# Optimization experiments

Hardware: AMD Instinct MI355X
Metric: run time of the kernel (lower is better)

The kernel has to match this reference:

```python
import jax, jax.numpy as jnp
import numpy as np

N_NODES = 100000


def gcn_conv(x, src, dst, W, b):
    # x: [N, F_in]; src/dst: [E'] (self-loops already appended)
    n = x.shape[0]
    deg = jax.ops.segment_sum(jnp.ones_like(src, dtype=x.dtype), dst, num_segments=n)
    dinv = jnp.where(deg > 0, jax.lax.rsqrt(deg), 0.0)
    norm = dinv[src] * dinv[dst]                      # [E']
    h = x @ W                                         # [N, F_out] (GEMM first: F_out small)
    msg = h[src] * norm[:, None]                      # gather + scale
    out = jax.ops.segment_sum(msg, dst, num_segments=n)  # scatter-add
    return out + b


def setup_inputs() -> dict:
    key = jax.random.key(0)
    k1, k2, k3, k4 = jax.random.split(key, 4)
    x = jax.random.normal(k1, (N_NODES, 1433), dtype=jnp.float32)
    edge_index = jax.random.randint(k2, (2, 3200000), 0, N_NODES, dtype=jnp.int32)
    W1 = jax.random.normal(k3, (1433, 32), dtype=jnp.float32) * (1.0 / np.sqrt(1433.0))
    b1 = jnp.zeros((32,), dtype=jnp.float32)
    W2 = jax.random.normal(k4, (32, 7), dtype=jnp.float32) * (1.0 / np.sqrt(32.0))
    b2 = jnp.zeros((7,), dtype=jnp.float32)
    return {"x": x, "edge_index": edge_index, "W1": W1, "b1": b1, "W2": W2, "b2": b2}


def reference(x, edge_index, W1, b1, W2, b2):
    n = x.shape[0]
    loop = jnp.arange(n, dtype=edge_index.dtype)      # add self-loops (GCNConv default)
    src = jnp.concatenate([edge_index[0], loop])
    dst = jnp.concatenate([edge_index[1], loop])
    h = gcn_conv(x, src, dst, W1, b1)
    h = jax.nn.relu(h)
    # F.dropout with training=False (eval mode) is identity
    h = gcn_conv(h, src, dst, W2, b2)
    return jax.nn.log_softmax(h, axis=1)
```

## Files before the change

kernel.cpp:

```cpp
#include <hip/hip_runtime.h>
#include <math.h>

#define F0 1433
#define F1 32
#define F2 7

__global__ void k_init_deg(float* __restrict__ deg, int N) {
    int i = blockIdx.x * 256 + threadIdx.x;
    if (i < N) deg[i] = 1.0f;
}

__global__ void k_count_deg(const int* __restrict__ dst, float* __restrict__ deg, int E) {
    int e = blockIdx.x * 256 + threadIdx.x;
    if (e < E) atomicAdd(&deg[dst[e]], 1.0f);
}

__global__ void k_dinv(float* __restrict__ deg, int N) {
    int i = blockIdx.x * 256 + threadIdx.x;
    if (i < N) deg[i] = rsqrtf(deg[i]);
}

#define BM 64
#define BK 64
#define XS_LD 68
__global__ __launch_bounds__(256) void k_gemm1(const float* __restrict__ x,
                                               const float* __restrict__ W,
                                               float* __restrict__ h, int N) {
    __shared__ float xs[BM * XS_LD];
    __shared__ float wsm[BK * F1];
    const int tid  = threadIdx.x;
    const int row0 = blockIdx.x * BM;
    const int cg   = tid & 7;
    const int r    = tid >> 3;

    float acc0x = 0.f, acc0y = 0.f, acc0z = 0.f, acc0w = 0.f;
    float acc1x = 0.f, acc1y = 0.f, acc1z = 0.f, acc1w = 0.f;

    for (int k0 = 0; k0 < F0; k0 += BK) {
        #pragma unroll
        for (int l = 0; l < 16; ++l) {
            int idx = tid + l * 256;
            int i = idx >> 6, j = idx & 63;
            int gr = row0 + i, gk = k0 + j;
            float v = 0.f;
            if (gr < N && gk < F0) v = x[(long)gr * F0 + gk];
            xs[i * XS_LD + j] = v;
        }
        #pragma unroll
        for (int l = 0; l < 8; ++l) {
            int idx = tid + l * 256;
            int kk = idx >> 5;
            int gk = k0 + kk;
            wsm[idx] = (gk < F0) ? W[gk * F1 + (idx & 31)] : 0.f;
        }
        __syncthreads();

        #pragma unroll
        for (int kk = 0; kk < BK; kk += 4) {
            float4 xa = *(const float4*)&xs[r * XS_LD + kk];
            float4 xb = *(const float4*)&xs[(r + 32) * XS_LD + kk];
            const float av[4] = {xa.x, xa.y, xa.z, xa.w};
            const float bv[4] = {xb.x, xb.y, xb.z, xb.w};
            #pragma unroll
            for (int u = 0; u < 4; ++u) {
                float4 w = *(const float4*)&wsm[(kk + u) * F1 + cg * 4];
                float a = av[u], b = bv[u];
                acc0x += a * w.x; acc0y += a * w.y; acc0z += a * w.z; acc0w += a * w.w;
                acc1x += b * w.x; acc1y += b * w.y; acc1z += b * w.z; acc1w += b * w.w;
            }
        }
        __syncthreads();
    }
    int gr0 = row0 + r, gr1 = row0 + r + 32;
    if (gr0 < N) *(float4*)&h[(long)gr0 * F1 + cg * 4] = make_float4(acc0x, acc0y, acc0z, acc0w);
    if (gr1 < N) *(float4*)&h[(long)gr1 * F1 + cg * 4] = make_float4(acc1x, acc1y, acc1z, acc1w);
}

__global__ void k_selfloop1(const float* __restrict__ h1, const float* __restrict__ dinv,
                            float* __restrict__ agg, int N) {
    int t = blockIdx.x * 256 + threadIdx.x;
    if (t < N * F1) {
        int i = t >> 5;
        float d = dinv[i];
        agg[t] = h1[t] * d * d;
    }
}

__global__ void k_scatter1(const int* __restrict__ src, const int* __restrict__ dst,
                           const float* __restrict__ dinv, const float* __restrict__ h1,
                           float* __restrict__ agg, int E) {
    int t = blockIdx.x * 256 + threadIdx.x;
    int e = t >> 5;
    if (e >= E) return;
    int f = t & 31;
    int s = src[e], d = dst[e];
    float w = dinv[s] * dinv[d];
    atomicAdd(&agg[d * F1 + f], h1[s * F1 + f] * w);
}

__global__ __launch_bounds__(256) void k_layer2(const float* __restrict__ agg1,
                                                const float* __restrict__ b1,
                                                const float* __restrict__ W2,
                                                const float* __restrict__ dinv,
                                                float* __restrict__ h2,
                                                float* __restrict__ out, int N) {
    __shared__ float w2s[F1 * F2];
    __shared__ float b1s[F1];
    int tid = threadIdx.x;
    if (tid < F1 * F2) w2s[tid] = W2[tid];
    if (tid < F1) b1s[tid] = b1[tid];
    __syncthreads();
    int i = blockIdx.x * 256 + tid;
    if (i >= N) return;
    float v[F1];
    #pragma unroll
    for (int u = 0; u < 8; ++u) {
        float4 t = *(const float4*)&agg1[(long)i * F1 + u * 4];
        v[u*4+0] = fmaxf(t.x + b1s[u*4+0], 0.f);
        v[u*4+1] = fmaxf(t.y + b1s[u*4+1], 0.f);
        v[u*4+2] = fmaxf(t.z + b1s[u*4+2], 0.f);
        v[u*4+3] = fmaxf(t.w + b1s[u*4+3], 0.f);
    }
    float o[F2] = {0.f, 0.f, 0.f, 0.f, 0.f, 0.f, 0.f};
    #pragma unroll
    for (int k = 0; k < F1; ++k) {
        float a = v[k];
        #pragma unroll
        for (int c = 0; c < F2; ++c) o[c] += a * w2s[k * F2 + c];
    }
    float di = dinv[i];
    float dd = di * di;
    #pragma unroll
    for (int c = 0; c < F2; ++c) {
        h2[(long)i * F2 + c] = o[c];
        out[(long)i * F2 + c] = o[c] * dd;
    }
}

__global__ void k_scatter2(const int* __restrict__ src, const int* __restrict__ dst,
                           const float* __restrict__ dinv, const float* __restrict__ h2,
                           float* __restrict__ out, int E) {
    int t = blockIdx.x * 256 + threadIdx.x;
    int e = t >> 3;
    int c = t & 7;
    if (e >= E || c >= F2) return;
    int s = src[e], d = dst[e];
    float w = dinv[s] * dinv[d];
    atomicAdd(&out[(long)d * F2 + c], h2[(long)s * F2 + c] * w);
}

__global__ void k_logsoftmax(float* __restrict__ out, const float* __restrict__ b2, int N) {
    int i = blockIdx.x * 256 + threadIdx.x;
    if (i >= N) return;
    float v[F2];
    float m = -1e30f;
    #pragma unroll
    for (int c = 0; c < F2; ++c) {
        v[c] = out[(long)i * F2 + c] + b2[c];
        m = fmaxf(m, v[c]);
    }
    float s = 0.f;
    #pragma unroll
    for (int c = 0; c < F2; ++c) s += expf(v[c] - m);
    float l = logf(s);
    #pragma unroll
    for (int c = 0; c < F2; ++c) out[(long)i * F2 + c] = v[c] - m - l;
}

extern "C" void kernel_launch(void* const* d_in, const int* in_sizes, int n_in,
                              void* d_out, int out_size, void* d_ws, size_t ws_size,
                              hipStream_t stream) {
    const float* x  = (const float*)d_in[0];
    const int*   ei = (const int*)d_in[1];
    const float* W1 = (const float*)d_in[2];
    const float* b1 = (const float*)d_in[3];
    const float* W2 = (const float*)d_in[4];
    const float* b2 = (const float*)d_in[5];
    float* out = (float*)d_out;

    const int N = in_sizes[0] / F0;
    const int E = in_sizes[1] / 2;
    const int* src = ei;
    const int* dst = ei + E;

    float* ws   = (float*)d_ws;
    size_t o    = 0;
    float* dinv = ws;        o += (size_t)((N + 3) & ~3);
    float* h1   = ws + o;    o += (size_t)N * F1;
    float* agg1 = ws + o;    o += (size_t)N * F1;
    float* h2   = h1;

    const int nb_N  = (N + 255) / 256;
    const int nb_E  = (E + 255) / 256;

    k_init_deg  <<<nb_N, 256, 0, stream>>>(dinv, N);
    k_count_deg <<<nb_E, 256, 0, stream>>>(dst, dinv, E);
    k_dinv      <<<nb_N, 256, 0, stream>>>(dinv, N);

    k_gemm1     <<<(N + BM - 1) / BM, 256, 0, stream>>>(x, W1, h1, N);

    k_selfloop1 <<<((size_t)N * F1 + 255) / 256, 256, 0, stream>>>(h1, dinv, agg1, N);
    k_scatter1  <<<((size_t)E * 32 + 255) / 256, 256, 0, stream>>>(src, dst, dinv, h1, agg1, E);

    k_layer2    <<<nb_N, 256, 0, stream>>>(agg1, b1, W2, dinv, h2, out, N);

    k_scatter2  <<<((size_t)E * 8 + 255) / 256, 256, 0, stream>>>(src, dst, dinv, h2, out, E);

    k_logsoftmax<<<nb_N, 256, 0, stream>>>(out, b2, N);
}
```

Before: 2.068 ms.

## Replace LDS-tiled layer-1 GEMM with direct-load GEMV and fuse self-loop init

Rewrites the first GEMM so each group of 8 threads computes one output row by streaming that row of x straight from global memory with float4 loads. W1 is read through the cache instead of being staged in shared memory, which removes the block barriers. The self-loop term (h scaled by dinv squared) is now written inside the GEMM epilogue, so the separate self-loop kernel and its extra pass over h1 are gone. The cost is less data reuse: x rows are no longer shared through LDS, the per-instruction access pattern is scattered, and float4 loads hit rows whose 1433-float stride is not 16-byte aligned.

```diff
diff --git a/kernel.cpp b/kernel.cpp
--- a/kernel.cpp
+++ b/kernel.cpp
@@ -20,70 +20,48 @@
     if (i < N) deg[i] = rsqrtf(deg[i]);
 }
 
-#define BM 64
-#define BK 64
-#define XS_LD 68
 __global__ __launch_bounds__(256) void k_gemm1(const float* __restrict__ x,
                                                const float* __restrict__ W,
-                                               float* __restrict__ h, int N) {
-    __shared__ float xs[BM * XS_LD];
-    __shared__ float wsm[BK * F1];
-    const int tid  = threadIdx.x;
-    const int row0 = blockIdx.x * BM;
-    const int cg   = tid & 7;
-    const int r    = tid >> 3;
+                                               const float* __restrict__ dinv,
+                                               float* __restrict__ h,
+                                               float* __restrict__ agg, int N) {
+    const int tid = threadIdx.x;
+    const int r   = blockIdx.x * 32 + (tid >> 3);
+    const int cg  = tid & 7;
+    if (r >= N) return;
 
-    float acc0x = 0.f, acc0y = 0.f, acc0z = 0.f, acc0w = 0.f;
-    float acc1x = 0.f, acc1y = 0.f, acc1z = 0.f, acc1w = 0.f;
+    const float* __restrict__ xr = x + (long)r * F0;
+    const float* __restrict__ wc = W + cg * 4;
 
-    for (int k0 = 0; k0 < F0; k0 += BK) {
+    float ax = 0.f, ay = 0.f, az = 0.f, aw = 0.f;
+
+    for (int k = 0; k < 1432; k += 8) {
+        float4 xa = *(const float4*)(xr + k);
+        float4 xb = *(const float4*)(xr + k + 4);
         #pragma unroll
-        for (int l = 0; l < 16; ++l) {
-            int idx = tid + l * 256;
-            int i = idx >> 6, j = idx & 63;
-            int gr = row0 + i, gk = k0 + j;
-            float v = 0.f;
-            if (gr < N && gk < F0) v = x[(long)gr * F0 + gk];
-            xs[i * XS_LD + j] = v;
+        for (int u = 0; u < 4; ++u) {
+            float4 w = *(const float4*)(wc + (long)(k + u) * F1);
+            float a = (u == 0) ? xa.x : (u == 1) ? xa.y : (u == 2) ? xa.z : xa.w;
+            ax += a * w.x; ay += a * w.y; az += a * w.z; aw += a * w.w;
         }
         #pragma unroll
-        for (int l = 0; l < 8; ++l) {
-            int idx = tid + l * 256;
-            int kk = idx >> 5;
-            int gk = k0 + kk;
-            wsm[idx] = (gk < F0) ? W[gk * F1 + (idx & 31)] : 0.f;
+        for (int u = 0; u < 4; ++u) {
+            float4 w = *(const float4*)(wc + (long)(k + 4 + u) * F1);
+            float a = (u == 0) ? xb.x : (u == 1) ? xb.y : (u == 2) ? xb.z : xb.w;
+            ax += a * w.x; ay += a * w.y; az += a * w.z; aw += a * w.w;
         }
-        __syncthreads();
+    }
+    {
+        float a = xr[1432];
+        float4 w = *(const float4*)(wc + (long)1432 * F1);
+        ax += a * w.x; ay += a * w.y; az += a * w.z; aw += a * w.w;
+    }
 
-        #pragma unroll
-        for (int kk = 0; kk < BK; kk += 4) {
-            float4 xa = *(const float4*)&xs[r * XS_LD + kk];
-            float4 xb = *(const float4*)&xs[(r + 32) * XS_LD + kk];
-            const float av[4] = {xa.x, xa.y, xa.z, xa.w};
-            const float bv[4] = {xb.x, xb.y, xb.z, xb.w};
-            #pragma unroll
-            for (int u = 0; u < 4; ++u) {
-                float4 w = *(const float4*)&wsm[(kk + u) * F1 + cg * 4];
-                float a = av[u], b = bv[u];
-                acc0x += a * w.x; acc0y += a * w.y; acc0z += a * w.z; acc0w += a * w.w;
-                acc1x += b * w.x; acc1y += b * w.y; acc1z += b * w.z; acc1w += b * w.w;
-            }
-        }
-        __syncthreads();
-    }
-    int gr0 = row0 + r, gr1 = row0 + r + 32;
-    if (gr0 < N) *(float4*)&h[(long)gr0 * F1 + cg * 4] = make_float4(acc0x, acc0y, acc0z, acc0w);
-    if (gr1 < N) *(float4*)&h[(long)gr1 * F1 + cg * 4] = make_float4(acc1x, acc1y, acc1z, acc1w);
-}
-
-__global__ void k_selfloop1(const float* __restrict__ h1, const float* __restrict__ dinv,
-                            float* __restrict__ agg, int N) {
-    int t = blockIdx.x * 256 + threadIdx.x;
-    if (t < N * F1) {
-        int i = t >> 5;
-        float d = dinv[i];
-        agg[t] = h1[t] * d * d;
-    }
+    float d  = dinv[r];
+    float dd = d * d;
+    long base = (long)r * F1 + cg * 4;
+    *(float4*)&h[base]   = make_float4(ax, ay, az, aw);
+    *(float4*)&agg[base] = make_float4(ax * dd, ay * dd, az * dd, aw * dd);
 }
 
 __global__ void k_scatter1(const int* __restrict__ src, const int* __restrict__ dst,
@@ -190,16 +168,15 @@
     float* agg1 = ws + o;    o += (size_t)N * F1;
     float* h2   = h1;
 
-    const int nb_N  = (N + 255) / 256;
-    const int nb_E  = (E + 255) / 256;
+    const int nb_N = (N + 255) / 256;
+    const int nb_E = (E + 255) / 256;
 
     k_init_deg  <<<nb_N, 256, 0, stream>>>(dinv, N);
     k_count_deg <<<nb_E, 256, 0, stream>>>(dst, dinv, E);
     k_dinv      <<<nb_N, 256, 0, stream>>>(dinv, N);
 
-    k_gemm1     <<<(N + BM - 1) / BM, 256, 0, stream>>>(x, W1, h1, N);
+    k_gemm1     <<<(N + 31) / 32, 256, 0, stream>>>(x, W1, dinv, h1, agg1, N);
 
-    k_selfloop1 <<<((size_t)N * F1 + 255) / 256, 256, 0, stream>>>(h1, dinv, agg1, N);
     k_scatter1  <<<((size_t)E * 32 + 255) / 256, 256, 0, stream>>>(src, dst, dinv, h1, agg1, E);
 
     k_layer2    <<<nb_N, 256, 0, stream>>>(agg1, b1, W2, dinv, h2, out, N);
```

New measurement: 2.185 ms. 1.06x slower.
